# Kernel optimization log

Hardware: AMD Instinct MI355X
Metric: run time of the kernel (lower is better)

Reference implementation:

```python
import jax, jax.numpy as jnp
import numpy as np

IN_C = 256
KEY_C = 256
VAL_C = 256
HEADS = 8


def setup_inputs() -> dict:
    key = jax.random.key(0)
    ks = jax.random.split(key, 9)
    s = 0.02
    return {
        "x": jax.random.normal(ks[0], (4, 8192, IN_C), dtype=jnp.float32),
        "Wk": jax.random.normal(ks[1], (KEY_C, IN_C), dtype=jnp.float32) * s,
        "bk": jax.random.normal(ks[2], (KEY_C,), dtype=jnp.float32) * s,
        "Wq": jax.random.normal(ks[3], (KEY_C, IN_C), dtype=jnp.float32) * s,
        "bq": jax.random.normal(ks[4], (KEY_C,), dtype=jnp.float32) * s,
        "Wv": jax.random.normal(ks[5], (VAL_C, IN_C), dtype=jnp.float32) * s,
        "bv": jax.random.normal(ks[6], (VAL_C,), dtype=jnp.float32) * s,
        "Wr": jax.random.normal(ks[7], (IN_C, VAL_C), dtype=jnp.float32) * s,
        "br": jax.random.normal(ks[8], (IN_C,), dtype=jnp.float32) * s,
    }


def reference(x, Wk, bk, Wq, bq, Wv, bv, Wr, br):
    n, N, c = x.shape
    # Faithful to torch: reshape (NOT transpose) of (n, N, c) into (n, c, N)
    xi = x.reshape(n, c, N)
    # 1x1 convs == channel-mixing matmuls over the token axis
    K = jnp.einsum('oc,ncs->nos', Wk, xi) + bk[None, :, None]
    Q = jnp.einsum('oc,ncs->nos', Wq, xi) + bq[None, :, None]
    V = jnp.einsum('oc,ncs->nos', Wv, xi) + bv[None, :, None]
    dk = KEY_C // HEADS
    dv = VAL_C // HEADS
    Kh = K.reshape(n, HEADS, dk, N)
    Qh = Q.reshape(n, HEADS, dk, N)
    Vh = V.reshape(n, HEADS, dv, N)
    # keys: softmax over tokens (dim=2); queries: softmax over head key channels (dim=1)
    Kh = jax.nn.softmax(Kh, axis=3)
    Qh = jax.nn.softmax(Qh, axis=2)
    # context = K @ V^T : [n, H, dk, dv]
    ctx = jnp.einsum('nhks,nhvs->nhkv', Kh, Vh)
    # attended = context^T @ Q : [n, H, dv, N]
    att = jnp.einsum('nhkv,nhks->nhvs', ctx, Qh)
    agg = att.reshape(n, VAL_C, N)
    rep = jnp.einsum('ov,nvs->nos', Wr, agg) + br[None, :, None]
    out = rep + xi  # residual in (n, c, N) layout
    return jnp.transpose(out, (0, 2, 1))  # (n, N, c)
```

## Files before the change

kernel.cpp:

```cpp
#include <hip/hip_runtime.h>

#define NTOK 8192
#define NCH  256
#define TT   64
#define XTP  264
#define EKP  72

typedef unsigned short u16;
typedef __attribute__((ext_vector_type(8))) short bf16x8;
typedef __attribute__((ext_vector_type(4))) float f32x4;
typedef __attribute__((ext_vector_type(8))) unsigned short u16x8;
typedef __attribute__((ext_vector_type(4))) unsigned short u16x4;

__device__ __forceinline__ float b2f(u16 h){
  union{unsigned u; float f;} x; x.u = ((unsigned)h) << 16; return x.f;
}
__device__ __forceinline__ u16 f2b(float f){
  union{float f; unsigned u;} x; x.f = f;
  unsigned u = x.u;
  return (u16)((u + 0x7FFFu + ((u >> 16) & 1u)) >> 16);
}
__device__ __forceinline__ f32x4 mfma16(bf16x8 a, bf16x8 b, f32x4 c){
  return __builtin_amdgcn_mfma_f32_16x16x32_bf16(a, b, c, 0, 0, 0);
}

__global__ __launch_bounds__(256)
void k_prep(const float* __restrict__ x,
            const float* __restrict__ Wk, const float* __restrict__ Wq,
            const float* __restrict__ Wv, const float* __restrict__ Wr,
            u16* __restrict__ xT, u16* __restrict__ wbf)
{
  __shared__ u16 ts[64 * 68];
  const int t = threadIdx.x, bid = blockIdx.x;
  if (bid < 2048) {
    const int b = bid >> 9, rem = bid & 511, tg = rem >> 2, cg = rem & 3;
    const float* xb = x + (size_t)b * NCH * NTOK;
    #pragma unroll
    for (int p = 0; p < 4; ++p) {
      int cl = p * 16 + (t >> 4);
      int tl = (t & 15) * 4;
      float4 v = *(const float4*)(xb + (size_t)(cg * 64 + cl) * NTOK + tg * 64 + tl);
      u16x4 pk; pk[0]=f2b(v.x); pk[1]=f2b(v.y); pk[2]=f2b(v.z); pk[3]=f2b(v.w);
      *(u16x4*)&ts[cl * 68 + tl] = pk;
    }
    __syncthreads();
    #pragma unroll
    for (int p = 0; p < 2; ++p) {
      int tl = p * 32 + (t >> 3);
      int cl = (t & 7) * 8;
      u16x8 o;
      #pragma unroll
      for (int j = 0; j < 8; ++j) o[j] = ts[(cl + j) * 68 + tl];
      *(u16x8*)(xT + (((size_t)(b * NTOK + tg * 64 + tl)) << 8) + cg * 64 + cl) = o;
    }
  } else {
    const int wb = bid - 2048;
    const int mat = wb >> 4;
    const float* src = (mat == 0) ? Wk : (mat == 1) ? Wq : (mat == 2) ? Wv : Wr;
    u16* dst = wbf + mat * 65536;
    const int base = (wb & 15) * 4096 + t * 16;
    #pragma unroll
    for (int i = 0; i < 4; ++i) {
      float4 v = *(const float4*)(src + base + i * 4);
      u16x4 pk; pk[0]=f2b(v.x); pk[1]=f2b(v.y); pk[2]=f2b(v.z); pk[3]=f2b(v.w);
      *(u16x4*)(dst + base + i * 4) = pk;
    }
  }
}

__global__ __launch_bounds__(512)
void k_ctx(const u16* __restrict__ xT, const u16* __restrict__ wbf,
           const float* __restrict__ bk, const float* __restrict__ bv,
           u16* __restrict__ ctxPart, float* __restrict__ denomPart)
{
  __shared__ u16 bufA[NCH * EKP];
  __shared__ u16 ekb[NCH * EKP];

  const int t = threadIdx.x;
  const int b = blockIdx.x >> 7, g = blockIdx.x & 127;
  const int w = t >> 6, lane = t & 63;
  const int l15 = lane & 15, quad = lane >> 4;
  const u16* Wkb = wbf;
  const u16* Wvb = wbf + 2 * 65536;

  {
    const u16* src = xT + ((size_t)(b * NTOK + g * TT) << 8);
    #pragma unroll
    for (int i = 0; i < 4; ++i) {
      int f = i * 4096 + t * 8;
      int tok = f >> 8, ch = f & 255;
      *(u16x8*)&bufA[tok * XTP + ch] = *(const u16x8*)(src + f);
    }
  }
  __syncthreads();

  f32x4 acc[2][4];

  #pragma unroll
  for (int mi = 0; mi < 2; ++mi)
    #pragma unroll
    for (int nj = 0; nj < 4; ++nj) acc[mi][nj] = (f32x4)0.f;
  for (int k0 = 0; k0 < NCH; k0 += 32) {
    bf16x8 af[2], bx[4];
    #pragma unroll
    for (int mi = 0; mi < 2; ++mi)
      af[mi] = *(const bf16x8*)(Wkb + (size_t)(w * 32 + mi * 16 + l15) * NCH + k0 + quad * 8);
    #pragma unroll
    for (int nj = 0; nj < 4; ++nj)
      bx[nj] = *(const bf16x8*)&bufA[(nj * 16 + l15) * XTP + k0 + quad * 8];
    #pragma unroll
    for (int mi = 0; mi < 2; ++mi)
      #pragma unroll
      for (int nj = 0; nj < 4; ++nj) acc[mi][nj] = mfma16(af[mi], bx[nj], acc[mi][nj]);
  }
  #pragma unroll
  for (int mi = 0; mi < 2; ++mi) {
    float4 bb = *(const float4*)(bk + w * 32 + mi * 16 + quad * 4);
    #pragma unroll
    for (int nj = 0; nj < 4; ++nj) {
      int tok = nj * 16 + l15, chb = w * 32 + mi * 16 + quad * 4;
      ekb[(chb + 0) * EKP + tok] = f2b(__expf(acc[mi][nj][0] + bb.x));
      ekb[(chb + 1) * EKP + tok] = f2b(__expf(acc[mi][nj][1] + bb.y));
      ekb[(chb + 2) * EKP + tok] = f2b(__expf(acc[mi][nj][2] + bb.z));
      ekb[(chb + 3) * EKP + tok] = f2b(__expf(acc[mi][nj][3] + bb.w));
    }
  }

  #pragma unroll
  for (int mi = 0; mi < 2; ++mi)
    #pragma unroll
    for (int nj = 0; nj < 4; ++nj) acc[mi][nj] = (f32x4)0.f;
  for (int k0 = 0; k0 < NCH; k0 += 32) {
    bf16x8 af[2], bx[4];
    #pragma unroll
    for (int mi = 0; mi < 2; ++mi)
      af[mi] = *(const bf16x8*)(Wvb + (size_t)(w * 32 + mi * 16 + l15) * NCH + k0 + quad * 8);
    #pragma unroll
    for (int nj = 0; nj < 4; ++nj)
      bx[nj] = *(const bf16x8*)&bufA[(nj * 16 + l15) * XTP + k0 + quad * 8];
    #pragma unroll
    for (int mi = 0; mi < 2; ++mi)
      #pragma unroll
      for (int nj = 0; nj < 4; ++nj) acc[mi][nj] = mfma16(af[mi], bx[nj], acc[mi][nj]);
  }
  __syncthreads();
  #pragma unroll
  for (int mi = 0; mi < 2; ++mi) {
    float4 bb = *(const float4*)(bv + w * 32 + mi * 16 + quad * 4);
    #pragma unroll
    for (int nj = 0; nj < 4; ++nj) {
      int tok = nj * 16 + l15, chb = w * 32 + mi * 16 + quad * 4;
      bufA[(chb + 0) * EKP + tok] = f2b(acc[mi][nj][0] + bb.x);
      bufA[(chb + 1) * EKP + tok] = f2b(acc[mi][nj][1] + bb.y);
      bufA[(chb + 2) * EKP + tok] = f2b(acc[mi][nj][2] + bb.z);
      bufA[(chb + 3) * EKP + tok] = f2b(acc[mi][nj][3] + bb.w);
    }
  }
  __syncthreads();

  f32x4 cacc[2][2];
  #pragma unroll
  for (int mi = 0; mi < 2; ++mi)
    #pragma unroll
    for (int nj = 0; nj < 2; ++nj) cacc[mi][nj] = (f32x4)0.f;
  #pragma unroll
  for (int kc = 0; kc < 2; ++kc) {
    bf16x8 ae[2], bvv[2];
    #pragma unroll
    for (int mi = 0; mi < 2; ++mi)
      ae[mi] = *(const bf16x8*)&ekb[(w * 32 + mi * 16 + l15) * EKP + kc * 32 + quad * 8];
    #pragma unroll
    for (int nj = 0; nj < 2; ++nj)
      bvv[nj] = *(const bf16x8*)&bufA[(w * 32 + nj * 16 + l15) * EKP + kc * 32 + quad * 8];
    #pragma unroll
    for (int mi = 0; mi < 2; ++mi)
      #pragma unroll
      for (int nj = 0; nj < 2; ++nj)
        cacc[mi][nj] = mfma16(ae[mi], bvv[nj], cacc[mi][nj]);
  }
  float dsum = 0.f;
  if (t < 256) {
    #pragma unroll
    for (int s = 0; s < TT; s += 8) {
      u16x8 v = *(const u16x8*)&ekb[t * EKP + s];
      #pragma unroll
      for (int j = 0; j < 8; ++j) dsum += b2f(v[j]);
    }
  }

  u16* cp = ctxPart + ((size_t)(b * 128 + g) << 13);
  #pragma unroll
  for (int mi = 0; mi < 2; ++mi)
    #pragma unroll
    for (int nj = 0; nj < 2; ++nj)
      #pragma unroll
      for (int r = 0; r < 4; ++r) {
        int e = ((w * 32 + mi * 16 + quad * 4 + r) << 5) + nj * 16 + l15;
        cp[e] = f2b(cacc[mi][nj][r]);
      }
  if (t < 256)
    denomPart[(size_t)(b * 128 + g) * 256 + t] = dsum;
}

__global__ __launch_bounds__(256)
void k_red(const u16* __restrict__ ctxPart, const float* __restrict__ denomPart,
           u16* __restrict__ ctxT, float* __restrict__ rdenomF)
{
  int i = blockIdx.x * 256 + threadIdx.x;
  if (i < 32768) {
    int b = i >> 13, e = i & 8191;
    const u16* p = ctxPart + ((size_t)(b * 128) << 13) + e;
    float s = 0.f;
    for (int g = 0; g < 128; ++g) s += b2f(p[(size_t)g << 13]);
    int hh = e >> 10, kk = (e >> 5) & 31, vch = e & 31;
    ctxT[(((b * 8 + hh) * 32 + vch) << 5) + kk] = f2b(s);
  } else if (i < 33792) {
    int j = i - 32768, b = j >> 8, ch = j & 255;
    const float* p = denomPart + (size_t)(b * 128) * 256 + ch;
    float s = 0.f;
    for (int g = 0; g < 128; ++g) s += p[(size_t)g << 8];
    rdenomF[j] = 1.0f / s;
  }
}

__global__ __launch_bounds__(512)
void k_out(const u16* __restrict__ xT, const u16* __restrict__ wbf,
           const float* __restrict__ bq, const float* __restrict__ br,
           const u16* __restrict__ ctxT, const float* __restrict__ rdenomF,
           float* __restrict__ out)
{
  __shared__ u16 xs[TT * XTP];
  __shared__ u16 qs[TT * XTP];

  const int t = threadIdx.x;
  const int b = blockIdx.x >> 7, g = blockIdx.x & 127;
  const int w = t >> 6, lane = t & 63;
  const int l15 = lane & 15, quad = lane >> 4;
  const u16* Wqb = wbf + 65536;
  const u16* Wrb = wbf + 3 * 65536;

  {
    const u16* src = xT + ((size_t)(b * NTOK + g * TT) << 8);
    #pragma unroll
    for (int i = 0; i < 4; ++i) {
      int f = i * 4096 + t * 8;
      int tok = f >> 8, ch = f & 255;
      *(u16x8*)&xs[tok * XTP + ch] = *(const u16x8*)(src + f);
    }
  }
  __syncthreads();

  f32x4 acc[2][4];
  #pragma unroll
  for (int mi = 0; mi < 2; ++mi)
    #pragma unroll
    for (int nj = 0; nj < 4; ++nj) acc[mi][nj] = (f32x4)0.f;
  for (int k0 = 0; k0 < NCH; k0 += 32) {
    bf16x8 af[2], bx[4];
    #pragma unroll
    for (int mi = 0; mi < 2; ++mi)
      af[mi] = *(const bf16x8*)(Wqb + (size_t)(w * 32 + mi * 16 + l15) * NCH + k0 + quad * 8);
    #pragma unroll
    for (int nj = 0; nj < 4; ++nj)
      bx[nj] = *(const bf16x8*)&xs[(nj * 16 + l15) * XTP + k0 + quad * 8];
    #pragma unroll
    for (int mi = 0; mi < 2; ++mi)
      #pragma unroll
      for (int nj = 0; nj < 4; ++nj) acc[mi][nj] = mfma16(af[mi], bx[nj], acc[mi][nj]);
  }
  #pragma unroll
  for (int mi = 0; mi < 2; ++mi) {
    float4 bb = *(const float4*)(bq + w * 32 + mi * 16 + quad * 4);
    #pragma unroll
    for (int nj = 0; nj < 4; ++nj) {
      acc[mi][nj][0] = __expf(acc[mi][nj][0] + bb.x);
      acc[mi][nj][1] = __expf(acc[mi][nj][1] + bb.y);
      acc[mi][nj][2] = __expf(acc[mi][nj][2] + bb.z);
      acc[mi][nj][3] = __expf(acc[mi][nj][3] + bb.w);
    }
  }
  float inv[4];
  #pragma unroll
  for (int nj = 0; nj < 4; ++nj) {
    float s = 0.f;
    #pragma unroll
    for (int mi = 0; mi < 2; ++mi)
      #pragma unroll
      for (int r = 0; r < 4; ++r) s += acc[mi][nj][r];
    s += __shfl_xor(s, 16);
    s += __shfl_xor(s, 32);
    inv[nj] = 1.0f / s;
  }
  #pragma unroll
  for (int mi = 0; mi < 2; ++mi) {
    float4 rd = *(const float4*)(rdenomF + b * 256 + w * 32 + mi * 16 + quad * 4);
    #pragma unroll
    for (int nj = 0; nj < 4; ++nj) {
      u16x4 pk;
      pk[0] = f2b(acc[mi][nj][0] * inv[nj] * rd.x);
      pk[1] = f2b(acc[mi][nj][1] * inv[nj] * rd.y);
      pk[2] = f2b(acc[mi][nj][2] * inv[nj] * rd.z);
      pk[3] = f2b(acc[mi][nj][3] * inv[nj] * rd.w);
      *(u16x4*)&qs[(nj * 16 + l15) * XTP + w * 32 + mi * 16 + quad * 4] = pk;
    }
  }
  __syncthreads();

  f32x4 aacc[2][4];
  {
    bf16x8 ac[2];
    #pragma unroll
    for (int mi = 0; mi < 2; ++mi)
      ac[mi] = *(const bf16x8*)(ctxT + (((size_t)(b * 8 + w) * 32 + mi * 16 + l15) << 5) + quad * 8);
    #pragma unroll
    for (int nj = 0; nj < 4; ++nj) {
      bf16x8 bqf = *(const bf16x8*)&qs[(nj * 16 + l15) * XTP + w * 32 + quad * 8];
      #pragma unroll
      for (int mi = 0; mi < 2; ++mi)
        aacc[mi][nj] = mfma16(ac[mi], bqf, (f32x4)0.f);
    }
  }
  #pragma unroll
  for (int mi = 0; mi < 2; ++mi)
    #pragma unroll
    for (int nj = 0; nj < 4; ++nj) {
      u16x4 pk;
      pk[0] = f2b(aacc[mi][nj][0]);
      pk[1] = f2b(aacc[mi][nj][1]);
      pk[2] = f2b(aacc[mi][nj][2]);
      pk[3] = f2b(aacc[mi][nj][3]);
      *(u16x4*)&qs[(nj * 16 + l15) * XTP + w * 32 + mi * 16 + quad * 4] = pk;
    }
  __syncthreads();

  #pragma unroll
  for (int mi = 0; mi < 2; ++mi)
    #pragma unroll
    for (int nj = 0; nj < 4; ++nj) acc[mi][nj] = (f32x4)0.f;
  for (int k0 = 0; k0 < NCH; k0 += 32) {
    bf16x8 af[2], bx[4];
    #pragma unroll
    for (int mi = 0; mi < 2; ++mi)
      af[mi] = *(const bf16x8*)(Wrb + (size_t)(w * 32 + mi * 16 + l15) * NCH + k0 + quad * 8);
    #pragma unroll
    for (int nj = 0; nj < 4; ++nj)
      bx[nj] = *(const bf16x8*)&qs[(nj * 16 + l15) * XTP + k0 + quad * 8];
    #pragma unroll
    for (int mi = 0; mi < 2; ++mi)
      #pragma unroll
      for (int nj = 0; nj < 4; ++nj) acc[mi][nj] = mfma16(af[mi], bx[nj], acc[mi][nj]);
  }
  #pragma unroll
  for (int mi = 0; mi < 2; ++mi) {
    float4 bb = *(const float4*)(br + w * 32 + mi * 16 + quad * 4);
    #pragma unroll
    for (int nj = 0; nj < 4; ++nj) {
      int tok = nj * 16 + l15;
      u16x4 rx = *(const u16x4*)&xs[tok * XTP + w * 32 + mi * 16 + quad * 4];
      float4 o;
      o.x = acc[mi][nj][0] + bb.x + b2f(rx[0]);
      o.y = acc[mi][nj][1] + bb.y + b2f(rx[1]);
      o.z = acc[mi][nj][2] + bb.z + b2f(rx[2]);
      o.w = acc[mi][nj][3] + bb.w + b2f(rx[3]);
      *(float4*)(out + (((size_t)(b * NTOK + g * TT + tok)) << 8) + w * 32 + mi * 16 + quad * 4) = o;
    }
  }
}

extern "C" void kernel_launch(void* const* d_in, const int* in_sizes, int n_in,
                              void* d_out, int out_size, void* d_ws, size_t ws_size,
                              hipStream_t stream) {
  const float* x  = (const float*)d_in[0];
  const float* Wk = (const float*)d_in[1];
  const float* bk = (const float*)d_in[2];
  const float* Wq = (const float*)d_in[3];
  const float* bq = (const float*)d_in[4];
  const float* Wv = (const float*)d_in[5];
  const float* bv = (const float*)d_in[6];
  const float* Wr = (const float*)d_in[7];
  const float* br = (const float*)d_in[8];
  float* out = (float*)d_out;

  char* wsb = (char*)d_ws;
  u16*   ctxPart   = (u16*)wsb;
  float* denomPart = (float*)(wsb + 8388608);
  u16*   ctxT      = (u16*)(wsb + 8912896);
  float* rdenomF   = (float*)(wsb + 8978432);
  u16*   wbf       = (u16*)(wsb + 8982528);
  u16*   xT        = (u16*)(wsb + 9506816);

  hipLaunchKernelGGL(k_prep, dim3(2112), dim3(256), 0, stream,
                     x, Wk, Wq, Wv, Wr, xT, wbf);
  hipLaunchKernelGGL(k_ctx, dim3(512), dim3(512), 0, stream,
                     xT, wbf, bk, bv, ctxPart, denomPart);
  hipLaunchKernelGGL(k_red, dim3(132), dim3(256), 0, stream,
                     ctxPart, denomPart, ctxT, rdenomF);
  hipLaunchKernelGGL(k_out, dim3(512), dim3(512), 0, stream,
                     xT, wbf, bq, br, ctxT, rdenomF, out);
}
```

Before: 150.3 us.

## Fuse x transpose into ctx/out kernels and replace reduction kernel with atomics

Drops the separate pass that converts and transposes x into a bf16 token-major buffer. The ctx and out kernels now load fp32 x directly and transpose it through shared memory. The partial-context reduction kernel is also removed: ctx blocks atomically add fp32 partials into a zeroed accumulator, and the out kernel computes the reciprocal denominators and the bf16 context fragments itself. This saves one full read and write of x plus a kernel launch, at the cost of atomic contention (128 blocks per batch), non-deterministic summation order, and doubled fp32 reads of x in two kernels.

```diff
diff --git a/kernel.cpp b/kernel.cpp
--- a/kernel.cpp
+++ b/kernel.cpp
@@ -24,54 +24,62 @@
   return __builtin_amdgcn_mfma_f32_16x16x32_bf16(a, b, c, 0, 0, 0);
 }
 
+__device__ __forceinline__ void stage_xtile(const float* __restrict__ xb,
+                                            u16* scratch, u16* dst, int t)
+{
+  #pragma unroll
+  for (int i = 0; i < 4; ++i) {
+    int ch = i * 64 + (t >> 3);
+    int tk = (t & 7) * 8;
+    const float* p = xb + (size_t)ch * NTOK + tk;
+    float4 v0 = *(const float4*)p;
+    float4 v1 = *(const float4*)(p + 4);
+    u16x8 pk;
+    pk[0]=f2b(v0.x); pk[1]=f2b(v0.y); pk[2]=f2b(v0.z); pk[3]=f2b(v0.w);
+    pk[4]=f2b(v1.x); pk[5]=f2b(v1.y); pk[6]=f2b(v1.z); pk[7]=f2b(v1.w);
+    *(u16x8*)&scratch[ch * EKP + tk] = pk;
+  }
+  __syncthreads();
+  #pragma unroll
+  for (int p = 0; p < 4; ++p) {
+    int idx = p * 512 + t;
+    int tok = idx & 63;
+    int ch = (idx >> 6) * 8;
+    u16x8 o;
+    #pragma unroll
+    for (int j = 0; j < 8; ++j) o[j] = scratch[(ch + j) * EKP + tok];
+    *(u16x8*)&dst[tok * XTP + ch] = o;
+  }
+}
+
 __global__ __launch_bounds__(256)
-void k_prep(const float* __restrict__ x,
-            const float* __restrict__ Wk, const float* __restrict__ Wq,
+void k_prep(const float* __restrict__ Wk, const float* __restrict__ Wq,
             const float* __restrict__ Wv, const float* __restrict__ Wr,
-            u16* __restrict__ xT, u16* __restrict__ wbf)
+            u16* __restrict__ wbf, float* __restrict__ ctxAcc)
 {
-  __shared__ u16 ts[64 * 68];
   const int t = threadIdx.x, bid = blockIdx.x;
-  if (bid < 2048) {
-    const int b = bid >> 9, rem = bid & 511, tg = rem >> 2, cg = rem & 3;
-    const float* xb = x + (size_t)b * NCH * NTOK;
-    #pragma unroll
-    for (int p = 0; p < 4; ++p) {
-      int cl = p * 16 + (t >> 4);
-      int tl = (t & 15) * 4;
-      float4 v = *(const float4*)(xb + (size_t)(cg * 64 + cl) * NTOK + tg * 64 + tl);
-      u16x4 pk; pk[0]=f2b(v.x); pk[1]=f2b(v.y); pk[2]=f2b(v.z); pk[3]=f2b(v.w);
-      *(u16x4*)&ts[cl * 68 + tl] = pk;
-    }
-    __syncthreads();
-    #pragma unroll
-    for (int p = 0; p < 2; ++p) {
-      int tl = p * 32 + (t >> 3);
-      int cl = (t & 7) * 8;
-      u16x8 o;
-      #pragma unroll
-      for (int j = 0; j < 8; ++j) o[j] = ts[(cl + j) * 68 + tl];
-      *(u16x8*)(xT + (((size_t)(b * NTOK + tg * 64 + tl)) << 8) + cg * 64 + cl) = o;
-    }
-  } else {
-    const int wb = bid - 2048;
-    const int mat = wb >> 4;
+  if (bid < 64) {
+    const int mat = bid >> 4;
     const float* src = (mat == 0) ? Wk : (mat == 1) ? Wq : (mat == 2) ? Wv : Wr;
     u16* dst = wbf + mat * 65536;
-    const int base = (wb & 15) * 4096 + t * 16;
+    const int base = (bid & 15) * 4096 + t * 16;
     #pragma unroll
     for (int i = 0; i < 4; ++i) {
       float4 v = *(const float4*)(src + base + i * 4);
       u16x4 pk; pk[0]=f2b(v.x); pk[1]=f2b(v.y); pk[2]=f2b(v.z); pk[3]=f2b(v.w);
       *(u16x4*)(dst + base + i * 4) = pk;
     }
-  }
-}
-
-__global__ __launch_bounds__(512)
-void k_ctx(const u16* __restrict__ xT, const u16* __restrict__ wbf,
+  } else {
+    int j = (bid - 64) * 1024 + t * 4;
+    float4 z; z.x = z.y = z.z = z.w = 0.f;
+    *(float4*)(ctxAcc + j) = z;
+  }
+}
+
+__global__ __launch_bounds__(512, 4)
+void k_ctx(const float* __restrict__ x, const u16* __restrict__ wbf,
            const float* __restrict__ bk, const float* __restrict__ bv,
-           u16* __restrict__ ctxPart, float* __restrict__ denomPart)
+           float* __restrict__ ctxAcc, float* __restrict__ denomAcc)
 {
   __shared__ u16 bufA[NCH * EKP];
   __shared__ u16 ekb[NCH * EKP];
@@ -83,15 +91,7 @@
   const u16* Wkb = wbf;
   const u16* Wvb = wbf + 2 * 65536;
 
-  {
-    const u16* src = xT + ((size_t)(b * NTOK + g * TT) << 8);
-    #pragma unroll
-    for (int i = 0; i < 4; ++i) {
-      int f = i * 4096 + t * 8;
-      int tok = f >> 8, ch = f & 255;
-      *(u16x8*)&bufA[tok * XTP + ch] = *(const u16x8*)(src + f);
-    }
-  }
+  stage_xtile(x + (size_t)b * NCH * NTOK + g * TT, ekb, bufA, t);
   __syncthreads();
 
   f32x4 acc[2][4];
@@ -188,7 +188,7 @@
     }
   }
 
-  u16* cp = ctxPart + ((size_t)(b * 128 + g) << 13);
+  float* cp = ctxAcc + ((size_t)b << 13);
   #pragma unroll
   for (int mi = 0; mi < 2; ++mi)
     #pragma unroll
@@ -196,41 +196,20 @@
       #pragma unroll
       for (int r = 0; r < 4; ++r) {
         int e = ((w * 32 + mi * 16 + quad * 4 + r) << 5) + nj * 16 + l15;
-        cp[e] = f2b(cacc[mi][nj][r]);
+        atomicAdd(&cp[e], cacc[mi][nj][r]);
       }
   if (t < 256)
-    denomPart[(size_t)(b * 128 + g) * 256 + t] = dsum;
-}
-
-__global__ __launch_bounds__(256)
-void k_red(const u16* __restrict__ ctxPart, const float* __restrict__ denomPart,
-           u16* __restrict__ ctxT, float* __restrict__ rdenomF)
-{
-  int i = blockIdx.x * 256 + threadIdx.x;
-  if (i < 32768) {
-    int b = i >> 13, e = i & 8191;
-    const u16* p = ctxPart + ((size_t)(b * 128) << 13) + e;
-    float s = 0.f;
-    for (int g = 0; g < 128; ++g) s += b2f(p[(size_t)g << 13]);
-    int hh = e >> 10, kk = (e >> 5) & 31, vch = e & 31;
-    ctxT[(((b * 8 + hh) * 32 + vch) << 5) + kk] = f2b(s);
-  } else if (i < 33792) {
-    int j = i - 32768, b = j >> 8, ch = j & 255;
-    const float* p = denomPart + (size_t)(b * 128) * 256 + ch;
-    float s = 0.f;
-    for (int g = 0; g < 128; ++g) s += p[(size_t)g << 8];
-    rdenomF[j] = 1.0f / s;
-  }
-}
-
-__global__ __launch_bounds__(512)
-void k_out(const u16* __restrict__ xT, const u16* __restrict__ wbf,
+    atomicAdd(&denomAcc[b * 256 + t], dsum);
+}
+
+__global__ __launch_bounds__(512, 4)
+void k_out(const float* __restrict__ x, const u16* __restrict__ wbf,
            const float* __restrict__ bq, const float* __restrict__ br,
-           const u16* __restrict__ ctxT, const float* __restrict__ rdenomF,
+           const float* __restrict__ ctxAcc, const float* __restrict__ denomAcc,
            float* __restrict__ out)
 {
   __shared__ u16 xs[TT * XTP];
-  __shared__ u16 qs[TT * XTP];
+  __shared__ u16 qs[NCH * EKP];
 
   const int t = threadIdx.x;
   const int b = blockIdx.x >> 7, g = blockIdx.x & 127;
@@ -239,16 +218,16 @@
   const u16* Wqb = wbf + 65536;
   const u16* Wrb = wbf + 3 * 65536;
 
-  {
-    const u16* src = xT + ((size_t)(b * NTOK + g * TT) << 8);
-    #pragma unroll
-    for (int i = 0; i < 4; ++i) {
-      int f = i * 4096 + t * 8;
-      int tok = f >> 8, ch = f & 255;
-      *(u16x8*)&xs[tok * XTP + ch] = *(const u16x8*)(src + f);
-    }
-  }
-  __syncthreads();
+  stage_xtile(x + (size_t)b * NCH * NTOK + g * TT, qs, xs, t);
+  __syncthreads();
+
+  const float* cb = ctxAcc + ((size_t)b << 13) + ((size_t)w << 10);
+  bf16x8 ac[2];
+  #pragma unroll
+  for (int mi = 0; mi < 2; ++mi)
+    #pragma unroll
+    for (int j = 0; j < 8; ++j)
+      ac[mi][j] = (short)f2b(cb[(quad * 8 + j) * 32 + mi * 16 + l15]);
 
   f32x4 acc[2][4];
   #pragma unroll
@@ -293,14 +272,15 @@
   }
   #pragma unroll
   for (int mi = 0; mi < 2; ++mi) {
-    float4 rd = *(const float4*)(rdenomF + b * 256 + w * 32 + mi * 16 + quad * 4);
+    float4 dv = *(const float4*)(denomAcc + b * 256 + w * 32 + mi * 16 + quad * 4);
+    float rdx = 1.0f / dv.x, rdy = 1.0f / dv.y, rdz = 1.0f / dv.z, rdw = 1.0f / dv.w;
     #pragma unroll
     for (int nj = 0; nj < 4; ++nj) {
       u16x4 pk;
-      pk[0] = f2b(acc[mi][nj][0] * inv[nj] * rd.x);
-      pk[1] = f2b(acc[mi][nj][1] * inv[nj] * rd.y);
-      pk[2] = f2b(acc[mi][nj][2] * inv[nj] * rd.z);
-      pk[3] = f2b(acc[mi][nj][3] * inv[nj] * rd.w);
+      pk[0] = f2b(acc[mi][nj][0] * inv[nj] * rdx);
+      pk[1] = f2b(acc[mi][nj][1] * inv[nj] * rdy);
+      pk[2] = f2b(acc[mi][nj][2] * inv[nj] * rdz);
+      pk[3] = f2b(acc[mi][nj][3] * inv[nj] * rdw);
       *(u16x4*)&qs[(nj * 16 + l15) * XTP + w * 32 + mi * 16 + quad * 4] = pk;
     }
   }
@@ -308,10 +288,6 @@
 
   f32x4 aacc[2][4];
   {
-    bf16x8 ac[2];
-    #pragma unroll
-    for (int mi = 0; mi < 2; ++mi)
-      ac[mi] = *(const bf16x8*)(ctxT + (((size_t)(b * 8 + w) * 32 + mi * 16 + l15) << 5) + quad * 8);
     #pragma unroll
     for (int nj = 0; nj < 4; ++nj) {
       bf16x8 bqf = *(const bf16x8*)&qs[(nj * 16 + l15) * XTP + w * 32 + quad * 8];
@@ -382,19 +358,14 @@
   float* out = (float*)d_out;
 
   char* wsb = (char*)d_ws;
-  u16*   ctxPart   = (u16*)wsb;
-  float* denomPart = (float*)(wsb + 8388608);
-  u16*   ctxT      = (u16*)(wsb + 8912896);
-  float* rdenomF   = (float*)(wsb + 8978432);
-  u16*   wbf       = (u16*)(wsb + 8982528);
-  u16*   xT        = (u16*)(wsb + 9506816);
-
-  hipLaunchKernelGGL(k_prep, dim3(2112), dim3(256), 0, stream,
-                     x, Wk, Wq, Wv, Wr, xT, wbf);
+  float* ctxAcc   = (float*)wsb;
+  float* denomAcc = (float*)(wsb + 131072);
+  u16*   wbf      = (u16*)(wsb + 135168);
+
+  hipLaunchKernelGGL(k_prep, dim3(97), dim3(256), 0, stream,
+                     Wk, Wq, Wv, Wr, wbf, ctxAcc);
   hipLaunchKernelGGL(k_ctx, dim3(512), dim3(512), 0, stream,
-                     xT, wbf, bk, bv, ctxPart, denomPart);
-  hipLaunchKernelGGL(k_red, dim3(132), dim3(256), 0, stream,
-                     ctxPart, denomPart, ctxT, rdenomF);
+                     x, wbf, bk, bv, ctxAcc, denomAcc);
   hipLaunchKernelGGL(k_out, dim3(512), dim3(512), 0, stream,
-                     xT, wbf, bq, br, ctxT, rdenomF, out);
-}
+                     x, wbf, bq, br, ctxAcc, denomAcc, out);
+}
```

Result: no change. 150.9 us (+0.4%).
